# Optimization experiments

Hardware: AMD Instinct MI355X
Metric: run time of the kernel (lower is better)

The kernel has to match this reference:

```python
import jax, jax.numpy as jnp
import numpy as np

B, T, C = 4, 1024, 1024
H, K, P = 16, 31, 15  # heads, kernel_size, padding_l
R = C // H

def setup_inputs() -> dict:
    key = jax.random.key(0)
    k1, k2 = jax.random.split(key)
    x = jax.random.normal(k1, (B, T, C), dtype=jnp.float32)
    # weight_linear: nn.Linear(n_in, H*K), no bias. torch layout: (out, in)
    W = jax.random.normal(k2, (H * K, C), dtype=jnp.float32) * 0.02
    return {"x": x, "W": W}

def reference(x, W):
    # dynamic per-position filters: (B,T,H,K)
    w = jnp.einsum('btc,kc->btk', x, W).reshape(B, T, H, K)
    # weight_softmax=True, renorm_padding=False: softmax over K in fp32
    w = jax.nn.softmax(w.astype(jnp.float32), axis=-1).astype(x.dtype)
    # depthwise band conv: out[b,t,h,r] = sum_k w[b,t,h,k] * x_pad[b, t+k, h, r]
    x_pad = jnp.pad(x, ((0, 0), (P, K - 1 - P), (0, 0)))
    # windows: (B,T,C,K) -- gather of K shifted views instead of O(T^2) band matrix
    x_unf = jnp.stack([x_pad[:, k:k + T, :] for k in range(K)], axis=-1)
    x_unf = x_unf.reshape(B, T, H, R, K)
    out = jnp.einsum('bthrk,bthk->bthr', x_unf, w)
    return out.reshape(B, T, C)
```

## Files before the change

kernel.cpp:

```cpp
#include <hip/hip_runtime.h>
#include <stdint.h>

typedef __attribute__((ext_vector_type(4))) float f32x4;
typedef __attribute__((ext_vector_type(8))) short short8;
typedef __attribute__((ext_vector_type(4))) unsigned short u16x4;

#define BB 4
#define TT 1024
#define CC 1024
#define HH 16
#define KSZ 31
#define PADL 15
#define RR 64
#define NL 496
#define NP 512
#define MM 4096

__device__ __forceinline__ unsigned short f2bf(float f) {
    uint32_t u = __float_as_uint(f);
    u += 0x7FFFu + ((u >> 16) & 1u);
    return (unsigned short)(u >> 16);
}

__device__ __forceinline__ void gload_lds16(const void* g, void* l) {
    __builtin_amdgcn_global_load_lds(
        (const __attribute__((address_space(1))) unsigned int*)g,
        (__attribute__((address_space(3))) unsigned int*)l, 16, 0, 0);
}

__device__ __forceinline__ int opaque_zero() {
    int zr = 0;
    asm volatile("" : "+v"(zr));
    return zr;
}

__global__ __launch_bounds__(256) void cast_kernel(const float* __restrict__ X,
                                                   const float* __restrict__ W,
                                                   unsigned short* __restrict__ Xb,
                                                   unsigned short* __restrict__ Wb,
                                                   int reps) {
    for (int rep = 0; rep < reps; ++rep) {
        const int i = blockIdx.x * 256 + threadIdx.x + opaque_zero();
        const int nx4 = MM * CC / 4;
        const int nw4 = NP * CC / 4;
        if (i < nx4) {
            f32x4 v = ((const f32x4*)X)[i];
            u16x4 o = { f2bf(v[0]), f2bf(v[1]), f2bf(v[2]), f2bf(v[3]) };
            ((u16x4*)Xb)[i] = o;
        } else if (i < nx4 + nw4) {
            const int j = i - nx4;
            const int n = j >> 8;
            u16x4 o = { 0, 0, 0, 0 };
            if (n < NL) {
                f32x4 v = ((const f32x4*)W)[j];
                o[0] = f2bf(v[0]); o[1] = f2bf(v[1]); o[2] = f2bf(v[2]); o[3] = f2bf(v[3]);
            }
            ((u16x4*)Wb)[j] = o;
        }
    }
}

__global__ __launch_bounds__(256) void gemm_mfma(const unsigned short* __restrict__ Xb,
                                                 const unsigned short* __restrict__ Wb,
                                                 float* __restrict__ LT,
                                                 int reps) {
    __shared__ unsigned short As[2 * 64 * 64];
    __shared__ unsigned short Bs[2 * 64 * 64];

    const int tid = threadIdx.x;
    const int lane = tid & 63;
    const int wv = tid >> 6;
    const int wm = wv >> 1, wn = wv & 1;

    int bid = blockIdx.x;
    bid = (bid & 7) * 64 + (bid >> 3);
    const int n0b = (bid & 7) * 64;
    const int m0b = (bid >> 3) * 64;

#define STAGE(ktt, bufsel) do {                                                  \
        const int k0s = (ktt) * 64;                                              \
        _Pragma("unroll")                                                        \
        for (int p = 0; p < 2; ++p) {                                            \
            const int c = p * 256 + tid;                                         \
            const int row = c >> 3, kcs = c & 7;                                 \
            const int kg = (kcs ^ (row & 7)) << 3;                               \
            gload_lds16(Xb + (size_t)(m0 + row) * CC + k0s + kg,                 \
                        (char*)As + (bufsel) * 8192 + c * 16);                   \
            gload_lds16(Wb + (size_t)(n0 + row) * CC + k0s + kg,                 \
                        (char*)Bs + (bufsel) * 8192 + c * 16);                   \
        }                                                                        \
    } while (0)

    for (int rep = 0; rep < reps; ++rep) {
        const int zr = opaque_zero();
        const int m0 = m0b + zr, n0 = n0b + zr;

        f32x4 acc[2][2] = {};
        int cur = 0;
        STAGE(0, 0);
        __syncthreads();

        for (int kt = 0; kt < CC / 64; ++kt) {
            if (kt + 1 < CC / 64) STAGE(kt + 1, cur ^ 1);
            const char* Ab = (const char*)As + cur * 8192;
            const char* Bb = (const char*)Bs + cur * 8192;
#pragma unroll
            for (int ks = 0; ks < 2; ++ks) {
                short8 af[2], bfv[2];
                const int kc = ks * 4 + (lane >> 4);
#pragma unroll
                for (int s = 0; s < 2; ++s) {
                    const int ra = wm * 32 + s * 16 + (lane & 15);
                    af[s] = *(const short8*)(Ab + ra * 128 + ((kc ^ (ra & 7)) << 4));
                    const int rb = wn * 32 + s * 16 + (lane & 15);
                    bfv[s] = *(const short8*)(Bb + rb * 128 + ((kc ^ (rb & 7)) << 4));
                }
#pragma unroll
                for (int si = 0; si < 2; ++si)
#pragma unroll
                    for (int sj = 0; sj < 2; ++sj)
                        acc[si][sj] = __builtin_amdgcn_mfma_f32_16x16x32_bf16(
                            af[si], bfv[sj], acc[si][sj], 0, 0, 0);
            }
            __syncthreads();
            cur ^= 1;
        }

        const int col = lane & 15, rbase = (lane >> 4) * 4;
#pragma unroll
        for (int si = 0; si < 2; ++si)
#pragma unroll
            for (int sj = 0; sj < 2; ++sj) {
                const int n = n0 + wn * 32 + sj * 16 + col;
                if (n < NL) {
                    const int m = m0 + wm * 32 + si * 16 + rbase;
                    *(f32x4*)&LT[(size_t)n * MM + m] = acc[si][sj];
                }
            }
        __syncthreads();
    }
#undef STAGE
}

__global__ __launch_bounds__(256) void conv_fused(const float* __restrict__ X,
                                                  const float* __restrict__ LT,
                                                  float* __restrict__ out,
                                                  int reps) {
    __shared__ float wsm[64 * 36];

    const int tid = threadIdx.x, lane = tid & 63, wv = tid >> 6;
    int bid = blockIdx.x;
    const int tt = bid & 15;
    const int h = (bid >> 4) & 15;
    const int b = bid >> 8;
    const int T0 = tt * 64;
    const int tlo = T0 + wv * 16 - PADL;

    for (int rep = 0; rep < reps; ++rep) {
        const int zr = opaque_zero();

        float xr[47];
#pragma unroll
        for (int rI = 0; rI < 46; ++rI) {
            const int tg = tlo + rI + zr;
            xr[rI] = ((unsigned)tg < TT)
                       ? X[(size_t)(b * TT + tg) * CC + h * RR + lane] : 0.f;
        }
        xr[46] = 0.f;

        const int j = lane & 3, a = lane >> 2;
        const int tl = wv * 16 + a;
        const int m = b * TT + T0 + tl;
        float v[8];
        float mx = -1e30f;
#pragma unroll
        for (int i = 0; i < 8; ++i) {
            const int kk = j * 8 + i;
            float lv = -1e30f;
            if (kk < KSZ) lv = LT[(size_t)(h * KSZ + kk) * MM + m];
            v[i] = lv; mx = fmaxf(mx, lv);
        }
        mx = fmaxf(mx, __shfl_xor(mx, 1));
        mx = fmaxf(mx, __shfl_xor(mx, 2));
        float s = 0.f;
#pragma unroll
        for (int i = 0; i < 8; ++i) { v[i] = __expf(v[i] - mx); s += v[i]; }
        s += __shfl_xor(s, 1);
        s += __shfl_xor(s, 2);
        const float inv = 1.f / s;
        f32x4 wlo = { v[0] * inv, v[1] * inv, v[2] * inv, v[3] * inv };
        f32x4 whi = { v[4] * inv, v[5] * inv, v[6] * inv, v[7] * inv };
        *(f32x4*)&wsm[tl * 36 + j * 8] = wlo;
        *(f32x4*)&wsm[tl * 36 + j * 8 + 4] = whi;
        __syncthreads();

        float acc[16];
#pragma unroll
        for (int t8 = 0; t8 < 16; ++t8) acc[t8] = 0.f;
#pragma unroll
        for (int t8 = 0; t8 < 16; ++t8) {
            const float* wp = &wsm[(wv * 16 + t8) * 36];
#pragma unroll
            for (int kq = 0; kq < 8; ++kq) {
                const f32x4 w4 = *(const f32x4*)(wp + kq * 4);
#pragma unroll
                for (int jj = 0; jj < 4; ++jj)
                    acc[t8] = fmaf(w4[jj], xr[t8 + kq * 4 + jj], acc[t8]);
            }
        }
#pragma unroll
        for (int t8 = 0; t8 < 16; ++t8)
            out[(size_t)(b * TT + T0 + wv * 16 + t8) * CC + h * RR + lane] = acc[t8];
        __syncthreads();
    }
}

extern "C" void kernel_launch(void* const* d_in, const int* in_sizes, int n_in,
                              void* d_out, int out_size, void* d_ws, size_t ws_size,
                              hipStream_t stream) {
    const float* x = (const float*)d_in[0];
    const float* W = (const float*)d_in[1];
    float* out = (float*)d_out;
    char* ws = (char*)d_ws;

    unsigned short* Xb = (unsigned short*)ws;
    unsigned short* Wb = (unsigned short*)(ws + 8388608);
    float* LT = (float*)(ws + 9437184);

    const int REPS = 1;

    cast_kernel<<<(MM * CC / 4 + NP * CC / 4 + 255) / 256, 256, 0, stream>>>(x, W, Xb, Wb, REPS);
    gemm_mfma<<<NP / 64 * (MM / 64), 256, 0, stream>>>(Xb, Wb, LT, REPS);
    conv_fused<<<BB * HH * (TT / 64), 256, 0, stream>>>(x, LT, out, REPS);
}
```

Measured before the change: 98.14 us.

## Fuse fp32-to-bf16 cast into GEMM staging via register prefetch

```diff
diff --git a/kernel.cpp b/kernel.cpp
--- a/kernel.cpp
+++ b/kernel.cpp
@@ -22,48 +22,9 @@
     return (unsigned short)(u >> 16);
 }
 
-__device__ __forceinline__ void gload_lds16(const void* g, void* l) {
-    __builtin_amdgcn_global_load_lds(
-        (const __attribute__((address_space(1))) unsigned int*)g,
-        (__attribute__((address_space(3))) unsigned int*)l, 16, 0, 0);
-}
-
-__device__ __forceinline__ int opaque_zero() {
-    int zr = 0;
-    asm volatile("" : "+v"(zr));
-    return zr;
-}
-
-__global__ __launch_bounds__(256) void cast_kernel(const float* __restrict__ X,
-                                                   const float* __restrict__ W,
-                                                   unsigned short* __restrict__ Xb,
-                                                   unsigned short* __restrict__ Wb,
-                                                   int reps) {
-    for (int rep = 0; rep < reps; ++rep) {
-        const int i = blockIdx.x * 256 + threadIdx.x + opaque_zero();
-        const int nx4 = MM * CC / 4;
-        const int nw4 = NP * CC / 4;
-        if (i < nx4) {
-            f32x4 v = ((const f32x4*)X)[i];
-            u16x4 o = { f2bf(v[0]), f2bf(v[1]), f2bf(v[2]), f2bf(v[3]) };
-            ((u16x4*)Xb)[i] = o;
-        } else if (i < nx4 + nw4) {
-            const int j = i - nx4;
-            const int n = j >> 8;
-            u16x4 o = { 0, 0, 0, 0 };
-            if (n < NL) {
-                f32x4 v = ((const f32x4*)W)[j];
-                o[0] = f2bf(v[0]); o[1] = f2bf(v[1]); o[2] = f2bf(v[2]); o[3] = f2bf(v[3]);
-            }
-            ((u16x4*)Wb)[j] = o;
-        }
-    }
-}
-
-__global__ __launch_bounds__(256) void gemm_mfma(const unsigned short* __restrict__ Xb,
-                                                 const unsigned short* __restrict__ Wb,
-                                                 float* __restrict__ LT,
-                                                 int reps) {
+__global__ __launch_bounds__(256) void gemm_fused(const float* __restrict__ X,
+                                                  const float* __restrict__ W,
+                                                  float* __restrict__ LT) {
     __shared__ unsigned short As[2 * 64 * 64];
     __shared__ unsigned short Bs[2 * 64 * 64];
 
@@ -74,78 +35,100 @@
 
     int bid = blockIdx.x;
     bid = (bid & 7) * 64 + (bid >> 3);
-    const int n0b = (bid & 7) * 64;
-    const int m0b = (bid >> 3) * 64;
-
-#define STAGE(ktt, bufsel) do {                                                  \
+    const int n0 = (bid & 7) * 64;
+    const int m0 = (bid >> 3) * 64;
+
+    int srow[4], saddr[4];
+#pragma unroll
+    for (int p = 0; p < 4; ++p) {
+        const int ch = p * 256 + tid;
+        const int row = ch >> 4, cc = ch & 15;
+        srow[p] = row;
+        saddr[p] = row * 128 + ((((cc >> 1) ^ (row & 7)) << 4) + ((cc & 1) << 3));
+    }
+
+#define LOADV(ktt, av, bv) do {                                                  \
         const int k0s = (ktt) * 64;                                              \
         _Pragma("unroll")                                                        \
-        for (int p = 0; p < 2; ++p) {                                            \
-            const int c = p * 256 + tid;                                         \
-            const int row = c >> 3, kcs = c & 7;                                 \
-            const int kg = (kcs ^ (row & 7)) << 3;                               \
-            gload_lds16(Xb + (size_t)(m0 + row) * CC + k0s + kg,                 \
-                        (char*)As + (bufsel) * 8192 + c * 16);                   \
-            gload_lds16(Wb + (size_t)(n0 + row) * CC + k0s + kg,                 \
-                        (char*)Bs + (bufsel) * 8192 + c * 16);                   \
+        for (int p = 0; p < 4; ++p) {                                            \
+            const int ch = p * 256 + tid;                                        \
+            const int cc = ch & 15;                                              \
+            av[p] = *(const f32x4*)&X[(size_t)(m0 + srow[p]) * CC + k0s + cc * 4]; \
+            const int n = n0 + srow[p];                                          \
+            bv[p] = (n < NL) ? *(const f32x4*)&W[(size_t)n * CC + k0s + cc * 4]  \
+                             : f32x4{0.f, 0.f, 0.f, 0.f};                        \
         }                                                                        \
     } while (0)
 
-    for (int rep = 0; rep < reps; ++rep) {
-        const int zr = opaque_zero();
-        const int m0 = m0b + zr, n0 = n0b + zr;
-
-        f32x4 acc[2][2] = {};
-        int cur = 0;
-        STAGE(0, 0);
+#define WRITEV(av, bv, bufsel) do {                                              \
+        _Pragma("unroll")                                                        \
+        for (int p = 0; p < 4; ++p) {                                            \
+            u16x4 ao = { f2bf(av[p][0]), f2bf(av[p][1]),                         \
+                         f2bf(av[p][2]), f2bf(av[p][3]) };                       \
+            u16x4 bo = { f2bf(bv[p][0]), f2bf(bv[p][1]),                         \
+                         f2bf(bv[p][2]), f2bf(bv[p][3]) };                       \
+            *(u16x4*)((char*)As + (bufsel) * 8192 + saddr[p]) = ao;              \
+            *(u16x4*)((char*)Bs + (bufsel) * 8192 + saddr[p]) = bo;              \
+        }                                                                        \
+    } while (0)
+
+    f32x4 acc[2][2] = {};
+    {
+        f32x4 a0[4], b0[4];
+        LOADV(0, a0, b0);
+        WRITEV(a0, b0, 0);
+    }
+    __syncthreads();
+
+    int cur = 0;
+    for (int kt = 0; kt < CC / 64; ++kt) {
+        f32x4 an[4], bn[4];
+        if (kt + 1 < CC / 64) LOADV(kt + 1, an, bn);
+
+        const char* Ab = (const char*)As + cur * 8192;
+        const char* Bb = (const char*)Bs + cur * 8192;
+#pragma unroll
+        for (int ks = 0; ks < 2; ++ks) {
+            short8 af[2], bfv[2];
+            const int kc = ks * 4 + (lane >> 4);
+#pragma unroll
+            for (int s = 0; s < 2; ++s) {
+                const int ra = wm * 32 + s * 16 + (lane & 15);
+                af[s] = *(const short8*)(Ab + ra * 128 + ((kc ^ (ra & 7)) << 4));
+                const int rb = wn * 32 + s * 16 + (lane & 15);
+                bfv[s] = *(const short8*)(Bb + rb * 128 + ((kc ^ (rb & 7)) << 4));
+            }
+#pragma unroll
+            for (int si = 0; si < 2; ++si)
+#pragma unroll
+                for (int sj = 0; sj < 2; ++sj)
+                    acc[si][sj] = __builtin_amdgcn_mfma_f32_16x16x32_bf16(
+                        af[si], bfv[sj], acc[si][sj], 0, 0, 0);
+        }
+
+        if (kt + 1 < CC / 64) WRITEV(an, bn, cur ^ 1);
         __syncthreads();
-
-        for (int kt = 0; kt < CC / 64; ++kt) {
-            if (kt + 1 < CC / 64) STAGE(kt + 1, cur ^ 1);
-            const char* Ab = (const char*)As + cur * 8192;
-            const char* Bb = (const char*)Bs + cur * 8192;
-#pragma unroll
-            for (int ks = 0; ks < 2; ++ks) {
-                short8 af[2], bfv[2];
-                const int kc = ks * 4 + (lane >> 4);
-#pragma unroll
-                for (int s = 0; s < 2; ++s) {
-                    const int ra = wm * 32 + s * 16 + (lane & 15);
-                    af[s] = *(const short8*)(Ab + ra * 128 + ((kc ^ (ra & 7)) << 4));
-                    const int rb = wn * 32 + s * 16 + (lane & 15);
-                    bfv[s] = *(const short8*)(Bb + rb * 128 + ((kc ^ (rb & 7)) << 4));
-                }
-#pragma unroll
-                for (int si = 0; si < 2; ++si)
-#pragma unroll
-                    for (int sj = 0; sj < 2; ++sj)
-                        acc[si][sj] = __builtin_amdgcn_mfma_f32_16x16x32_bf16(
-                            af[si], bfv[sj], acc[si][sj], 0, 0, 0);
+        cur ^= 1;
+    }
+#undef LOADV
+#undef WRITEV
+
+    const int col = lane & 15, rbase = (lane >> 4) * 4;
+#pragma unroll
+    for (int si = 0; si < 2; ++si)
+#pragma unroll
+        for (int sj = 0; sj < 2; ++sj) {
+            const int n = n0 + wn * 32 + sj * 16 + col;
+            if (n < NL) {
+                const int m = m0 + wm * 32 + si * 16 + rbase;
+                *(f32x4*)&LT[(size_t)n * MM + m] = acc[si][sj];
             }
-            __syncthreads();
-            cur ^= 1;
         }
-
-        const int col = lane & 15, rbase = (lane >> 4) * 4;
-#pragma unroll
-        for (int si = 0; si < 2; ++si)
-#pragma unroll
-            for (int sj = 0; sj < 2; ++sj) {
-                const int n = n0 + wn * 32 + sj * 16 + col;
-                if (n < NL) {
-                    const int m = m0 + wm * 32 + si * 16 + rbase;
-                    *(f32x4*)&LT[(size_t)n * MM + m] = acc[si][sj];
-                }
-            }
-        __syncthreads();
-    }
-#undef STAGE
 }
 
 __global__ __launch_bounds__(256) void conv_fused(const float* __restrict__ X,
                                                   const float* __restrict__ LT,
-                                                  float* __restrict__ out,
-                                                  int reps) {
+                                                  float* __restrict__ out) {
     __shared__ float wsm[64 * 36];
 
     const int tid = threadIdx.x, lane = tid & 63, wv = tid >> 6;
@@ -156,63 +139,58 @@
     const int T0 = tt * 64;
     const int tlo = T0 + wv * 16 - PADL;
 
-    for (int rep = 0; rep < reps; ++rep) {
-        const int zr = opaque_zero();
-
-        float xr[47];
-#pragma unroll
-        for (int rI = 0; rI < 46; ++rI) {
-            const int tg = tlo + rI + zr;
-            xr[rI] = ((unsigned)tg < TT)
-                       ? X[(size_t)(b * TT + tg) * CC + h * RR + lane] : 0.f;
+    float xr[47];
+#pragma unroll
+    for (int rI = 0; rI < 46; ++rI) {
+        const int tg = tlo + rI;
+        xr[rI] = ((unsigned)tg < TT)
+                   ? X[(size_t)(b * TT + tg) * CC + h * RR + lane] : 0.f;
+    }
+    xr[46] = 0.f;
+
+    const int j = lane & 3, a = lane >> 2;
+    const int tl = wv * 16 + a;
+    const int m = b * TT + T0 + tl;
+    float v[8];
+    float mx = -1e30f;
+#pragma unroll
+    for (int i = 0; i < 8; ++i) {
+        const int kk = j * 8 + i;
+        float lv = -1e30f;
+        if (kk < KSZ) lv = LT[(size_t)(h * KSZ + kk) * MM + m];
+        v[i] = lv; mx = fmaxf(mx, lv);
+    }
+    mx = fmaxf(mx, __shfl_xor(mx, 1));
+    mx = fmaxf(mx, __shfl_xor(mx, 2));
+    float s = 0.f;
+#pragma unroll
+    for (int i = 0; i < 8; ++i) { v[i] = __expf(v[i] - mx); s += v[i]; }
+    s += __shfl_xor(s, 1);
+    s += __shfl_xor(s, 2);
+    const float inv = 1.f / s;
+    f32x4 wlo = { v[0] * inv, v[1] * inv, v[2] * inv, v[3] * inv };
+    f32x4 whi = { v[4] * inv, v[5] * inv, v[6] * inv, v[7] * inv };
+    *(f32x4*)&wsm[tl * 36 + j * 8] = wlo;
+    *(f32x4*)&wsm[tl * 36 + j * 8 + 4] = whi;
+    __syncthreads();
+
+    float acc[16];
+#pragma unroll
+    for (int t8 = 0; t8 < 16; ++t8) acc[t8] = 0.f;
+#pragma unroll
+    for (int t8 = 0; t8 < 16; ++t8) {
+        const float* wp = &wsm[(wv * 16 + t8) * 36];
+#pragma unroll
+        for (int kq = 0; kq < 8; ++kq) {
+            const f32x4 w4 = *(const f32x4*)(wp + kq * 4);
+#pragma unroll
+            for (int jj = 0; jj < 4; ++jj)
+                acc[t8] = fmaf(w4[jj], xr[t8 + kq * 4 + jj], acc[t8]);
         }
-        xr[46] = 0.f;
-
-        const int j = lane & 3, a = lane >> 2;
-        const int tl = wv * 16 + a;
-        const int m = b * TT + T0 + tl;
-        float v[8];
-        float mx = -1e30f;
-#pragma unroll
-        for (int i = 0; i < 8; ++i) {
-            const int kk = j * 8 + i;
-            float lv = -1e30f;
-            if (kk < KSZ) lv = LT[(size_t)(h * KSZ + kk) * MM + m];
-            v[i] = lv; mx = fmaxf(mx, lv);
-        }
-        mx = fmaxf(mx, __shfl_xor(mx, 1));
-        mx = fmaxf(mx, __shfl_xor(mx, 2));
-        float s = 0.f;
-#pragma unroll
-        for (int i = 0; i < 8; ++i) { v[i] = __expf(v[i] - mx); s += v[i]; }
-        s += __shfl_xor(s, 1);
-        s += __shfl_xor(s, 2);
-        const float inv = 1.f / s;
-        f32x4 wlo = { v[0] * inv, v[1] * inv, v[2] * inv, v[3] * inv };
-        f32x4 whi = { v[4] * inv, v[5] * inv, v[6] * inv, v[7] * inv };
-        *(f32x4*)&wsm[tl * 36 + j * 8] = wlo;
-        *(f32x4*)&wsm[tl * 36 + j * 8 + 4] = whi;
-        __syncthreads();
-
-        float acc[16];
-#pragma unroll
-        for (int t8 = 0; t8 < 16; ++t8) acc[t8] = 0.f;
-#pragma unroll
-        for (int t8 = 0; t8 < 16; ++t8) {
-            const float* wp = &wsm[(wv * 16 + t8) * 36];
-#pragma unroll
-            for (int kq = 0; kq < 8; ++kq) {
-                const f32x4 w4 = *(const f32x4*)(wp + kq * 4);
-#pragma unroll
-                for (int jj = 0; jj < 4; ++jj)
-                    acc[t8] = fmaf(w4[jj], xr[t8 + kq * 4 + jj], acc[t8]);
-            }
-        }
-#pragma unroll
-        for (int t8 = 0; t8 < 16; ++t8)
-            out[(size_t)(b * TT + T0 + wv * 16 + t8) * CC + h * RR + lane] = acc[t8];
-        __syncthreads();
-    }
+    }
+#pragma unroll
+    for (int t8 = 0; t8 < 16; ++t8)
+        out[(size_t)(b * TT + T0 + wv * 16 + t8) * CC + h * RR + lane] = acc[t8];
 }
 
 extern "C" void kernel_launch(void* const* d_in, const int* in_sizes, int n_in,
@@ -221,15 +199,8 @@
     const float* x = (const float*)d_in[0];
     const float* W = (const float*)d_in[1];
     float* out = (float*)d_out;
-    char* ws = (char*)d_ws;
-
-    unsigned short* Xb = (unsigned short*)ws;
-    unsigned short* Wb = (unsigned short*)(ws + 8388608);
-    float* LT = (float*)(ws + 9437184);
-
-    const int REPS = 1;
-
-    cast_kernel<<<(MM * CC / 4 + NP * CC / 4 + 255) / 256, 256, 0, stream>>>(x, W, Xb, Wb, REPS);
-    gemm_mfma<<<NP / 64 * (MM / 64), 256, 0, stream>>>(Xb, Wb, LT, REPS);
-    conv_fused<<<BB * HH * (TT / 64), 256, 0, stream>>>(x, LT, out, REPS);
-}
+    float* LT = (float*)d_ws;
+
+    gemm_fused<<<NP / 64 * (MM / 64), 256, 0, stream>>>(x, W, LT);
+    conv_fused<<<BB * HH * (TT / 64), 256, 0, stream>>>(x, LT, out);
+}
```

Result: faster. 92.98 us (-5.3%).
